# Kernel tuning notes

Hardware: AMD Instinct MI355X
Metric: run time of the kernel (lower is better)

Reference implementation:

```python
import jax, jax.numpy as jnp
import numpy as np

EPS = 1e-6
NUM_HEADS = 16

def rmsnorm(x, w):
    # x: [..., d], w: [d]
    norm = jax.lax.rsqrt(jnp.mean(x * x, axis=-1, keepdims=True) + EPS)
    return w * (x * norm)

def setup_inputs() -> dict:
    key = jax.random.key(0)
    ks = jax.random.split(key, 6)
    B, N, C = 2, 2048, 1024
    H = NUM_HEADS
    hd = C // H
    x = jax.random.normal(ks[0], (B, N, C), dtype=jnp.float32)
    scale = 1.0 / np.sqrt(C)
    qkv_w = jax.random.normal(ks[1], (C, 3 * C), dtype=jnp.float32) * scale
    qkv_b = jnp.zeros((3 * C,), dtype=jnp.float32)
    q_norm_w = jnp.ones((hd,), dtype=jnp.float32)
    k_norm_w = jnp.ones((hd,), dtype=jnp.float32)
    proj_w = jax.random.normal(ks[2], (C, C), dtype=jnp.float32) * scale
    proj_b = jnp.zeros((C,), dtype=jnp.float32)
    return {"x": x, "qkv_w": qkv_w, "qkv_b": qkv_b,
            "q_norm_w": q_norm_w, "k_norm_w": k_norm_w,
            "proj_w": proj_w, "proj_b": proj_b}

def reference(x, qkv_w, qkv_b, q_norm_w, k_norm_w, proj_w, proj_b):
    B, N, C = x.shape
    H = NUM_HEADS
    hd = C // H
    qkv = x @ qkv_w + qkv_b                       # [B,N,3C]
    qkv = qkv.reshape(B, N, 3, H, hd)
    q, k, v = qkv[:, :, 0], qkv[:, :, 1], qkv[:, :, 2]  # [B,N,H,hd]
    q = jnp.transpose(q, (0, 2, 1, 3))            # [B,H,N,hd]
    k = jnp.transpose(k, (0, 2, 1, 3))
    v = jnp.transpose(v, (0, 2, 1, 3))
    q = rmsnorm(q, q_norm_w)
    k = rmsnorm(k, k_norm_w)
    scores = jnp.einsum('bhqd,bhkd->bhqk', q, k) / jnp.sqrt(jnp.float32(hd))
    attn = jax.nn.softmax(scores, axis=-1)
    out = jnp.einsum('bhqk,bhkd->bhqd', attn, v)  # [B,H,N,hd]
    out = jnp.transpose(out, (0, 2, 1, 3)).reshape(B, N, C)
    return out @ proj_w + proj_b
```

## Files before the change

kernel.cpp:

```cpp
#include <hip/hip_runtime.h>

typedef unsigned short u16;
typedef unsigned int u32;
typedef __bf16 bf16x8 __attribute__((ext_vector_type(8)));
typedef float f32x4 __attribute__((ext_vector_type(4)));
typedef unsigned short u16x8 __attribute__((ext_vector_type(8)));
typedef unsigned short u16x4 __attribute__((ext_vector_type(4)));
typedef float f4 __attribute__((ext_vector_type(4)));

__device__ __forceinline__ float bf2f(u16 u) {
    union { unsigned int i; float f; } c; c.i = ((unsigned int)u) << 16; return c.f;
}
__device__ __forceinline__ u16 f2bf(float f) {
    union { float f; unsigned int i; } c; c.f = f;
    unsigned int r = c.i + 0x7FFFu + ((c.i >> 16) & 1u);
    return (u16)(r >> 16);
}
__device__ __forceinline__ u16 f2bf_rtz(float f) {
    union { float f; unsigned int i; } c; c.f = f;
    return (u16)(c.i >> 16);
}
__device__ __forceinline__ float fast_exp2(float x) {
#if __has_builtin(__builtin_amdgcn_exp2f)
    return __builtin_amdgcn_exp2f(x);
#else
    return exp2f(x);
#endif
}
__device__ __forceinline__ void async16(const void* g, void* l) {
    __builtin_amdgcn_global_load_lds(
        (const __attribute__((address_space(1))) u32*)g,
        (__attribute__((address_space(3))) u32*)l, 16, 0, 0);
}

__global__ __launch_bounds__(256) void cast_bf16(
    const float* __restrict__ X, u16* __restrict__ H)
{
    const size_t i = ((size_t)blockIdx.x * 256 + threadIdx.x) * 8;
    u16x8 h;
    #pragma unroll
    for (int e = 0; e < 8; ++e) h[e] = f2bf(X[i + e]);
    *(u16x8*)&H[i] = h;
}

__global__ __launch_bounds__(256) void transpose_cast(
    const float* __restrict__ W, u16* __restrict__ Th, int K, int N)
{
    __shared__ float tile[32][33];
    const int bk = blockIdx.y * 32, bn = blockIdx.x * 32;
    const int tx = threadIdx.x & 31, ty = threadIdx.x >> 5;
    #pragma unroll
    for (int r = ty; r < 32; r += 8)
        tile[r][tx] = W[(size_t)(bk + r) * N + bn + tx];
    __syncthreads();
    #pragma unroll
    for (int r = ty; r < 32; r += 8)
        Th[(size_t)(bn + r) * K + bk + tx] = f2bf(tile[tx][r]);
}

template <int EPI>
__global__ __launch_bounds__(256) void gemm_fused(
    const u16* __restrict__ AH, const u16* __restrict__ BH,
    const float* __restrict__ bias, float* __restrict__ C,
    u16* __restrict__ Qb, u16* __restrict__ Kb, u16* __restrict__ Vt,
    const float* __restrict__ qw, const float* __restrict__ kw,
    int M, int N, int K)
{
    __shared__ __align__(16) u16 AhT[128 * 32];
    __shared__ __align__(16) u16 BhT[128 * 32];
    const int t = threadIdx.x;
    const int bm = blockIdx.y * 128, bn = blockIdx.x * 128;
    const int wave = t >> 6, lane = t & 63;
    const int wm = (wave >> 1) * 64, wn = (wave & 1) * 64;
    const int l15 = lane & 15, quad = lane >> 4;
    const int srow = lane >> 2, scol = (lane & 3) * 8;

    f32x4 acc[4][4];
    const f32x4 zero = {0.0f, 0.0f, 0.0f, 0.0f};
    #pragma unroll
    for (int i = 0; i < 4; ++i)
        #pragma unroll
        for (int j = 0; j < 4; ++j) acc[i][j] = zero;

    for (int k0 = 0; k0 < K; k0 += 32) {
        #pragma unroll
        for (int rr = 0; rr < 2; ++rr) {
            const int r0 = (rr * 4 + wave) * 16;
            const size_t ga = (size_t)(bm + r0 + srow) * K + k0 + scol;
            const size_t gb = (size_t)(bn + r0 + srow) * K + k0 + scol;
            async16(&AH[ga], &AhT[r0 * 32]);
            async16(&BH[gb], &BhT[r0 * 32]);
        }
        __syncthreads();
        bf16x8 ah[4], bh[4];
        #pragma unroll
        for (int i = 0; i < 4; ++i)
            ah[i] = *(const bf16x8*)&AhT[(wm + i * 16 + l15) * 32 + quad * 8];
        #pragma unroll
        for (int j = 0; j < 4; ++j)
            bh[j] = *(const bf16x8*)&BhT[(wn + j * 16 + l15) * 32 + quad * 8];
        #pragma unroll
        for (int i = 0; i < 4; ++i)
            #pragma unroll
            for (int j = 0; j < 4; ++j)
                acc[i][j] = __builtin_amdgcn_mfma_f32_16x16x32_bf16(
                    ah[i], bh[j], acc[i][j], 0, 0, 0);
        __syncthreads();
    }

    if (EPI == 1) {
        #pragma unroll
        for (int j = 0; j < 4; ++j) {
            const int col = bn + wn + j * 16 + l15;
            const float bv = bias[col];
            #pragma unroll
            for (int i = 0; i < 4; ++i) {
                const int row = bm + wm + i * 16 + quad * 4;
                #pragma unroll
                for (int r = 0; r < 4; ++r)
                    C[(size_t)(row + r) * N + col] = acc[i][j][r] + bv;
            }
        }
    } else {
        const int gc0 = bn + wn;
        const int sec = gc0 >> 10;
        const int h = (gc0 & 1023) >> 6;
        const int b = bm >> 11;
        const int bhd = b * 16 + h;
        float bv[4], wj[4];
        #pragma unroll
        for (int j = 0; j < 4; ++j) {
            const int d = j * 16 + l15;
            bv[j] = bias[gc0 + d];
            wj[j] = (sec == 2) ? 0.0f
                  : (sec ? kw[d] : qw[d] * 0.18033688011f);
        }
        if (sec < 2) {
            u16* dst = sec ? Kb : Qb;
            #pragma unroll
            for (int i = 0; i < 4; ++i) {
                float val[4][4];
                float ss[4] = {0.0f, 0.0f, 0.0f, 0.0f};
                #pragma unroll
                for (int j = 0; j < 4; ++j)
                    #pragma unroll
                    for (int r = 0; r < 4; ++r) {
                        val[j][r] = acc[i][j][r] + bv[j];
                        ss[r] += val[j][r] * val[j][r];
                    }
                #pragma unroll
                for (int r = 0; r < 4; ++r) {
                    #pragma unroll
                    for (int m = 1; m < 16; m <<= 1)
                        ss[r] += __shfl_xor(ss[r], m, 64);
                    const float nrm = rsqrtf(ss[r] * 0.015625f + 1e-6f);
                    const int n = (bm + wm + i * 16 + quad * 4 + r) & 2047;
                    const size_t rowb = ((size_t)bhd * 2048 + n) * 64;
                    #pragma unroll
                    for (int j = 0; j < 4; ++j)
                        dst[rowb + j * 16 + l15] = f2bf(val[j][r] * nrm * wj[j]);
                }
            }
        } else {
            #pragma unroll
            for (int i = 0; i < 4; ++i) {
                const int n0 = (bm + wm + i * 16 + quad * 4) & 2047;
                #pragma unroll
                for (int j = 0; j < 4; ++j) {
                    const int d = j * 16 + l15;
                    u16x4 pk;
                    #pragma unroll
                    for (int r = 0; r < 4; ++r)
                        pk[r] = f2bf(acc[i][j][r] + bv[j]);
                    *(u16x4*)&Vt[((size_t)bhd * 64 + d) * 2048 + n0] = pk;
                }
            }
        }
    }
}

__global__ __launch_bounds__(256) void flash_attn_mfma(
    const u16* __restrict__ Qb, const u16* __restrict__ Kb,
    const u16* __restrict__ Vt, u16* __restrict__ Attn)
{
    __shared__ __align__(16) u16 Qlds[128 * 64];
    __shared__ __align__(16) u16 Klds[64 * 64];
    __shared__ __align__(16) u16 Vlds[64 * 64];
    __shared__ u16 Plds[128][72];

    const int t = threadIdx.x;
    const int qt = blockIdx.x;
    const int bh = blockIdx.y;
    const int n0 = qt * 128;
    const size_t qbase = ((size_t)bh * 2048 + n0) * 64;
    const size_t kbase = (size_t)bh * 2048 * 64;
    const size_t vbase = (size_t)bh * 64 * 2048;
    const int wave = t >> 6, lane = t & 63;
    const int l15 = lane & 15, quad = lane >> 4;
    const int srow8 = lane >> 3;
    const int sgrp = lane & 7;

    #pragma unroll
    for (int c = 0; c < 4; ++c) {
        const int r0 = wave * 32 + c * 8;
        const int row = r0 + srow8;
        const int gg = sgrp ^ (row & 7);
        async16(&Qb[qbase + (size_t)row * 64 + gg * 8], &Qlds[r0 * 64]);
    }
    __syncthreads();

    int kofs[4][2];
    #pragma unroll
    for (int nt = 0; nt < 4; ++nt) {
        const int row = nt * 16 + l15;
        kofs[nt][0] = row * 64 + ((quad ^ (row & 7)) * 8);
        kofs[nt][1] = row * 64 + (((quad + 4) ^ (row & 7)) * 8);
    }
    bf16x8 qf[2][2];
    #pragma unroll
    for (int qs = 0; qs < 2; ++qs) {
        const int row = wave * 32 + qs * 16 + l15;
        qf[qs][0] = *(const bf16x8*)&Qlds[row * 64 + ((quad ^ (row & 7)) * 8)];
        qf[qs][1] = *(const bf16x8*)&Qlds[row * 64 + (((quad + 4) ^ (row & 7)) * 8)];
    }

    f32x4 o[2][4];
    const f32x4 zero = {0.0f, 0.0f, 0.0f, 0.0f};
    #pragma unroll
    for (int qs = 0; qs < 2; ++qs)
        #pragma unroll
        for (int dt = 0; dt < 4; ++dt) o[qs][dt] = zero;
    float lsum[2][4] = {};

    for (int kt = 0; kt < 32; ++kt) {
        __syncthreads();
        #pragma unroll
        for (int cc = 0; cc < 2; ++cc) {
            const int r0 = (wave + cc * 4) * 8;
            const int row = r0 + srow8;
            const int gg = sgrp ^ (row & 7);
            async16(&Kb[kbase + (size_t)(kt * 64 + row) * 64 + gg * 8],
                    &Klds[r0 * 64]);
            async16(&Vt[vbase + (size_t)row * 2048 + kt * 64 + gg * 8],
                    &Vlds[r0 * 64]);
        }
        __syncthreads();

        f32x4 s[2][4];
        #pragma unroll
        for (int nt = 0; nt < 4; ++nt) {
            bf16x8 kf0 = *(const bf16x8*)&Klds[kofs[nt][0]];
            bf16x8 kf1 = *(const bf16x8*)&Klds[kofs[nt][1]];
            #pragma unroll
            for (int qs = 0; qs < 2; ++qs) {
                s[qs][nt] = zero;
                s[qs][nt] = __builtin_amdgcn_mfma_f32_16x16x32_bf16(
                    qf[qs][0], kf0, s[qs][nt], 0, 0, 0);
                s[qs][nt] = __builtin_amdgcn_mfma_f32_16x16x32_bf16(
                    qf[qs][1], kf1, s[qs][nt], 0, 0, 0);
            }
        }

        #pragma unroll
        for (int qs = 0; qs < 2; ++qs) {
            const int prow = wave * 32 + qs * 16 + quad * 4;
            #pragma unroll
            for (int nt = 0; nt < 4; ++nt)
                #pragma unroll
                for (int r = 0; r < 4; ++r) {
                    const float p = fast_exp2(s[qs][nt][r]);
                    lsum[qs][r] += p;
                    Plds[prow + r][nt * 16 + l15] = f2bf_rtz(p);
                }
        }

        bf16x8 pf[2][2];
        #pragma unroll
        for (int qs = 0; qs < 2; ++qs) {
            const int prow = wave * 32 + qs * 16 + l15;
            pf[qs][0] = *(const bf16x8*)&Plds[prow][quad * 8];
            pf[qs][1] = *(const bf16x8*)&Plds[prow][quad * 8 + 32];
        }

        #pragma unroll
        for (int dt = 0; dt < 4; ++dt) {
            bf16x8 vf0 = *(const bf16x8*)&Vlds[kofs[dt][0]];
            bf16x8 vf1 = *(const bf16x8*)&Vlds[kofs[dt][1]];
            #pragma unroll
            for (int qs = 0; qs < 2; ++qs) {
                o[qs][dt] = __builtin_amdgcn_mfma_f32_16x16x32_bf16(
                    pf[qs][0], vf0, o[qs][dt], 0, 0, 0);
                o[qs][dt] = __builtin_amdgcn_mfma_f32_16x16x32_bf16(
                    pf[qs][1], vf1, o[qs][dt], 0, 0, 0);
            }
        }
    }

    #pragma unroll
    for (int qs = 0; qs < 2; ++qs)
        #pragma unroll
        for (int r = 0; r < 4; ++r) {
            #pragma unroll
            for (int m = 1; m < 16; m <<= 1)
                lsum[qs][r] += __shfl_xor(lsum[qs][r], m, 64);
        }
    const size_t obase =
        ((size_t)(bh >> 4) * 2048 + n0) * 1024 + (bh & 15) * 64;
    #pragma unroll
    for (int qs = 0; qs < 2; ++qs)
        #pragma unroll
        for (int r = 0; r < 4; ++r) {
            const float inv = 1.0f / lsum[qs][r];
            const size_t rbase =
                obase + (size_t)(wave * 32 + qs * 16 + quad * 4 + r) * 1024;
            #pragma unroll
            for (int dt = 0; dt < 4; ++dt)
                Attn[rbase + dt * 16 + l15] = f2bf(o[qs][dt][r] * inv);
        }
}

extern "C" void kernel_launch(void* const* d_in, const int* in_sizes, int n_in,
                              void* d_out, int out_size, void* d_ws, size_t ws_size,
                              hipStream_t stream)
{
    const float* x      = (const float*)d_in[0];
    const float* qkv_w  = (const float*)d_in[1];
    const float* qkv_b  = (const float*)d_in[2];
    const float* q_nw   = (const float*)d_in[3];
    const float* k_nw   = (const float*)d_in[4];
    const float* proj_w = (const float*)d_in[5];
    const float* proj_b = (const float*)d_in[6];
    float* out = (float*)d_out;

    char* ws = (char*)d_ws;
    u16* AttnB = (u16*)ws;
    u16* qwT   = (u16*)(ws + 8388608);
    u16* pwT   = (u16*)(ws + 14680064);
    u16* Xb    = (u16*)(ws + 16777216);
    u16* QbB   = (u16*)(ws + 25165824);
    u16* KbB   = (u16*)(ws + 33554432);
    u16* VtB   = (u16*)(ws + 41943040);
    (void)in_sizes; (void)n_in; (void)out_size;
    if (ws_size < 50331648u) return;

    cast_bf16<<<dim3(2048), 256, 0, stream>>>(x, Xb);
    transpose_cast<<<dim3(3072 / 32, 1024 / 32), 256, 0, stream>>>(
        qkv_w, qwT, 1024, 3072);
    transpose_cast<<<dim3(1024 / 32, 1024 / 32), 256, 0, stream>>>(
        proj_w, pwT, 1024, 1024);
    gemm_fused<0><<<dim3(3072 / 128, 4096 / 128), 256, 0, stream>>>(
        Xb, qwT, qkv_b, nullptr, QbB, KbB, VtB, q_nw, k_nw, 4096, 3072, 1024);
    flash_attn_mfma<<<dim3(16, 32), 256, 0, stream>>>(QbB, KbB, VtB, AttnB);
    gemm_fused<1><<<dim3(1024 / 128, 4096 / 128), 256, 0, stream>>>(
        AttnB, pwT, proj_b, out, nullptr, nullptr, nullptr, nullptr, nullptr,
        4096, 1024, 1024);
}
```

Measured before the change: 226.2 us.

## Split attention over two key halves and shrink projection GEMM tiles

Flash attention now splits the key sequence into two halves along a new grid z dimension. Each half writes unnormalized fp32 partial outputs and row sums, and a new combine kernel adds them, normalizes and casts to bf16. This doubles the number of attention blocks so the 256 CUs get more concurrent work. The projection GEMM is split out with a 64x128 tile, doubling its block count for the same reason. The cost is extra fp32 partial-output traffic, one more kernel launch and a larger workspace. The combine is only correct because the softmax does no running-max rescaling, which appears to rely on normalized q/k keeping scores bounded.

```diff
diff --git a/kernel.cpp b/kernel.cpp
--- a/kernel.cpp
+++ b/kernel.cpp
@@ -58,14 +58,13 @@
         Th[(size_t)(bn + r) * K + bk + tx] = f2bf(tile[tx][r]);
 }
 
-template <int EPI>
-__global__ __launch_bounds__(256) void gemm_fused(
+__global__ __launch_bounds__(256) void gemm_qkv(
     const u16* __restrict__ AH, const u16* __restrict__ BH,
-    const float* __restrict__ bias, float* __restrict__ C,
+    const float* __restrict__ bias,
     u16* __restrict__ Qb, u16* __restrict__ Kb, u16* __restrict__ Vt,
-    const float* __restrict__ qw, const float* __restrict__ kw,
-    int M, int N, int K)
-{
+    const float* __restrict__ qw, const float* __restrict__ kw)
+{
+    const int M = 4096, N = 3072, K = 1024; (void)M; (void)N;
     __shared__ __align__(16) u16 AhT[128 * 32];
     __shared__ __align__(16) u16 BhT[128 * 32];
     const int t = threadIdx.x;
@@ -108,80 +107,129 @@
         __syncthreads();
     }
 
-    if (EPI == 1) {
-        #pragma unroll
-        for (int j = 0; j < 4; ++j) {
-            const int col = bn + wn + j * 16 + l15;
-            const float bv = bias[col];
-            #pragma unroll
-            for (int i = 0; i < 4; ++i) {
-                const int row = bm + wm + i * 16 + quad * 4;
+    const int gc0 = bn + wn;
+    const int sec = gc0 >> 10;
+    const int h = (gc0 & 1023) >> 6;
+    const int b = bm >> 11;
+    const int bhd = b * 16 + h;
+    float bv[4], wj[4];
+    #pragma unroll
+    for (int j = 0; j < 4; ++j) {
+        const int d = j * 16 + l15;
+        bv[j] = bias[gc0 + d];
+        wj[j] = (sec == 2) ? 0.0f : (sec ? kw[d] : qw[d] * 0.18033688011f);
+    }
+    if (sec < 2) {
+        u16* dst = sec ? Kb : Qb;
+        #pragma unroll
+        for (int i = 0; i < 4; ++i) {
+            float val[4][4];
+            float ss[4] = {0.0f, 0.0f, 0.0f, 0.0f};
+            #pragma unroll
+            for (int j = 0; j < 4; ++j)
+                #pragma unroll
+                for (int r = 0; r < 4; ++r) {
+                    val[j][r] = acc[i][j][r] + bv[j];
+                    ss[r] += val[j][r] * val[j][r];
+                }
+            #pragma unroll
+            for (int r = 0; r < 4; ++r) {
+                #pragma unroll
+                for (int m = 1; m < 16; m <<= 1)
+                    ss[r] += __shfl_xor(ss[r], m, 64);
+                const float nrm = rsqrtf(ss[r] * 0.015625f + 1e-6f);
+                const int n = (bm + wm + i * 16 + quad * 4 + r) & 2047;
+                const size_t rowb = ((size_t)bhd * 2048 + n) * 64;
+                #pragma unroll
+                for (int j = 0; j < 4; ++j)
+                    dst[rowb + j * 16 + l15] = f2bf(val[j][r] * nrm * wj[j]);
+            }
+        }
+    } else {
+        #pragma unroll
+        for (int i = 0; i < 4; ++i) {
+            const int n0 = (bm + wm + i * 16 + quad * 4) & 2047;
+            #pragma unroll
+            for (int j = 0; j < 4; ++j) {
+                const int d = j * 16 + l15;
+                u16x4 pk;
                 #pragma unroll
                 for (int r = 0; r < 4; ++r)
-                    C[(size_t)(row + r) * N + col] = acc[i][j][r] + bv;
+                    pk[r] = f2bf(acc[i][j][r] + bv[j]);
+                *(u16x4*)&Vt[((size_t)bhd * 64 + d) * 2048 + n0] = pk;
             }
         }
-    } else {
-        const int gc0 = bn + wn;
-        const int sec = gc0 >> 10;
-        const int h = (gc0 & 1023) >> 6;
-        const int b = bm >> 11;
-        const int bhd = b * 16 + h;
-        float bv[4], wj[4];
-        #pragma unroll
-        for (int j = 0; j < 4; ++j) {
-            const int d = j * 16 + l15;
-            bv[j] = bias[gc0 + d];
-            wj[j] = (sec == 2) ? 0.0f
-                  : (sec ? kw[d] : qw[d] * 0.18033688011f);
-        }
-        if (sec < 2) {
-            u16* dst = sec ? Kb : Qb;
-            #pragma unroll
-            for (int i = 0; i < 4; ++i) {
-                float val[4][4];
-                float ss[4] = {0.0f, 0.0f, 0.0f, 0.0f};
-                #pragma unroll
-                for (int j = 0; j < 4; ++j)
-                    #pragma unroll
-                    for (int r = 0; r < 4; ++r) {
-                        val[j][r] = acc[i][j][r] + bv[j];
-                        ss[r] += val[j][r] * val[j][r];
-                    }
-                #pragma unroll
-                for (int r = 0; r < 4; ++r) {
-                    #pragma unroll
-                    for (int m = 1; m < 16; m <<= 1)
-                        ss[r] += __shfl_xor(ss[r], m, 64);
-                    const float nrm = rsqrtf(ss[r] * 0.015625f + 1e-6f);
-                    const int n = (bm + wm + i * 16 + quad * 4 + r) & 2047;
-                    const size_t rowb = ((size_t)bhd * 2048 + n) * 64;
-                    #pragma unroll
-                    for (int j = 0; j < 4; ++j)
-                        dst[rowb + j * 16 + l15] = f2bf(val[j][r] * nrm * wj[j]);
-                }
-            }
-        } else {
-            #pragma unroll
-            for (int i = 0; i < 4; ++i) {
-                const int n0 = (bm + wm + i * 16 + quad * 4) & 2047;
-                #pragma unroll
-                for (int j = 0; j < 4; ++j) {
-                    const int d = j * 16 + l15;
-                    u16x4 pk;
-                    #pragma unroll
-                    for (int r = 0; r < 4; ++r)
-                        pk[r] = f2bf(acc[i][j][r] + bv[j]);
-                    *(u16x4*)&Vt[((size_t)bhd * 64 + d) * 2048 + n0] = pk;
-                }
-            }
+    }
+}
+
+__global__ __launch_bounds__(256) void gemm_proj(
+    const u16* __restrict__ AH, const u16* __restrict__ BH,
+    const float* __restrict__ bias, float* __restrict__ C)
+{
+    const int N = 1024, K = 1024;
+    __shared__ __align__(16) u16 AhT[64 * 32];
+    __shared__ __align__(16) u16 BhT[128 * 32];
+    const int t = threadIdx.x;
+    const int bm = blockIdx.y * 64, bn = blockIdx.x * 128;
+    const int wave = t >> 6, lane = t & 63;
+    const int l15 = lane & 15, quad = lane >> 4;
+    const int srow = lane >> 2, scol = (lane & 3) * 8;
+
+    f32x4 acc[4][2];
+    const f32x4 zero = {0.0f, 0.0f, 0.0f, 0.0f};
+    #pragma unroll
+    for (int i = 0; i < 4; ++i)
+        #pragma unroll
+        for (int j = 0; j < 2; ++j) acc[i][j] = zero;
+
+    for (int k0 = 0; k0 < K; k0 += 32) {
+        {
+            const int r0 = wave * 16;
+            async16(&AH[(size_t)(bm + r0 + srow) * K + k0 + scol],
+                    &AhT[r0 * 32]);
+        }
+        #pragma unroll
+        for (int cc = 0; cc < 2; ++cc) {
+            const int r0 = (wave * 2 + cc) * 16;
+            async16(&BH[(size_t)(bn + r0 + srow) * K + k0 + scol],
+                    &BhT[r0 * 32]);
+        }
+        __syncthreads();
+        bf16x8 ah[4], bh[2];
+        #pragma unroll
+        for (int i = 0; i < 4; ++i)
+            ah[i] = *(const bf16x8*)&AhT[(i * 16 + l15) * 32 + quad * 8];
+        #pragma unroll
+        for (int j = 0; j < 2; ++j)
+            bh[j] = *(const bf16x8*)
+                &BhT[(wave * 32 + j * 16 + l15) * 32 + quad * 8];
+        #pragma unroll
+        for (int i = 0; i < 4; ++i)
+            #pragma unroll
+            for (int j = 0; j < 2; ++j)
+                acc[i][j] = __builtin_amdgcn_mfma_f32_16x16x32_bf16(
+                    ah[i], bh[j], acc[i][j], 0, 0, 0);
+        __syncthreads();
+    }
+
+    #pragma unroll
+    for (int j = 0; j < 2; ++j) {
+        const int col = bn + wave * 32 + j * 16 + l15;
+        const float bv = bias[col];
+        #pragma unroll
+        for (int i = 0; i < 4; ++i) {
+            const int row = bm + i * 16 + quad * 4;
+            #pragma unroll
+            for (int r = 0; r < 4; ++r)
+                C[(size_t)(row + r) * N + col] = acc[i][j][r] + bv;
         }
     }
 }
 
 __global__ __launch_bounds__(256) void flash_attn_mfma(
     const u16* __restrict__ Qb, const u16* __restrict__ Kb,
-    const u16* __restrict__ Vt, u16* __restrict__ Attn)
+    const u16* __restrict__ Vt, float* __restrict__ Opart,
+    float* __restrict__ Lpart)
 {
     __shared__ __align__(16) u16 Qlds[128 * 64];
     __shared__ __align__(16) u16 Klds[64 * 64];
@@ -191,6 +239,7 @@
     const int t = threadIdx.x;
     const int qt = blockIdx.x;
     const int bh = blockIdx.y;
+    const int z = blockIdx.z;
     const int n0 = qt * 128;
     const size_t qbase = ((size_t)bh * 2048 + n0) * 64;
     const size_t kbase = (size_t)bh * 2048 * 64;
@@ -232,16 +281,17 @@
         for (int dt = 0; dt < 4; ++dt) o[qs][dt] = zero;
     float lsum[2][4] = {};
 
-    for (int kt = 0; kt < 32; ++kt) {
+    for (int kt = 0; kt < 16; ++kt) {
+        const int ktG = z * 16 + kt;
         __syncthreads();
         #pragma unroll
         for (int cc = 0; cc < 2; ++cc) {
             const int r0 = (wave + cc * 4) * 8;
             const int row = r0 + srow8;
             const int gg = sgrp ^ (row & 7);
-            async16(&Kb[kbase + (size_t)(kt * 64 + row) * 64 + gg * 8],
+            async16(&Kb[kbase + (size_t)(ktG * 64 + row) * 64 + gg * 8],
                     &Klds[r0 * 64]);
-            async16(&Vt[vbase + (size_t)row * 2048 + kt * 64 + gg * 8],
+            async16(&Vt[vbase + (size_t)row * 2048 + ktG * 64 + gg * 8],
                     &Vlds[r0 * 64]);
         }
         __syncthreads();
@@ -304,19 +354,43 @@
             for (int m = 1; m < 16; m <<= 1)
                 lsum[qs][r] += __shfl_xor(lsum[qs][r], m, 64);
         }
+    const int b = bh >> 4, h = bh & 15;
     const size_t obase =
-        ((size_t)(bh >> 4) * 2048 + n0) * 1024 + (bh & 15) * 64;
+        ((size_t)z * 4096 + b * 2048 + n0) * 1024 + h * 64;
+    const size_t lbase = (size_t)z * 32 * 2048 + (size_t)bh * 2048 + n0;
     #pragma unroll
     for (int qs = 0; qs < 2; ++qs)
         #pragma unroll
         for (int r = 0; r < 4; ++r) {
-            const float inv = 1.0f / lsum[qs][r];
-            const size_t rbase =
-                obase + (size_t)(wave * 32 + qs * 16 + quad * 4 + r) * 1024;
+            const int rofs = wave * 32 + qs * 16 + quad * 4 + r;
+            if (l15 == 0) Lpart[lbase + rofs] = lsum[qs][r];
+            const size_t rbase = obase + (size_t)rofs * 1024;
             #pragma unroll
             for (int dt = 0; dt < 4; ++dt)
-                Attn[rbase + dt * 16 + l15] = f2bf(o[qs][dt][r] * inv);
-        }
+                Opart[rbase + dt * 16 + l15] = o[qs][dt][r];
+        }
+}
+
+__global__ __launch_bounds__(256) void attn_combine(
+    const float* __restrict__ Opart, const float* __restrict__ Lpart,
+    u16* __restrict__ Attn)
+{
+    const int row = blockIdx.x;
+    const int t = threadIdx.x;
+    const int col = t * 4;
+    const int b = row >> 11, n = row & 2047;
+    const int h = col >> 6;
+    const int bh = b * 16 + h;
+    const float l0 = Lpart[(size_t)bh * 2048 + n];
+    const float l1 = Lpart[65536 + (size_t)bh * 2048 + n];
+    const float inv = 1.0f / (l0 + l1);
+    const size_t idx = (size_t)row * 1024 + col;
+    f4 o0 = *(const f4*)&Opart[idx];
+    f4 o1 = *(const f4*)&Opart[4194304 + idx];
+    u16x4 pk;
+    #pragma unroll
+    for (int e = 0; e < 4; ++e) pk[e] = f2bf((o0[e] + o1[e]) * inv);
+    *(u16x4*)&Attn[idx] = pk;
 }
 
 extern "C" void kernel_launch(void* const* d_in, const int* in_sizes, int n_in,
@@ -333,25 +407,28 @@
     float* out = (float*)d_out;
 
     char* ws = (char*)d_ws;
-    u16* AttnB = (u16*)ws;
-    u16* qwT   = (u16*)(ws + 8388608);
-    u16* pwT   = (u16*)(ws + 14680064);
-    u16* Xb    = (u16*)(ws + 16777216);
-    u16* QbB   = (u16*)(ws + 25165824);
-    u16* KbB   = (u16*)(ws + 33554432);
-    u16* VtB   = (u16*)(ws + 41943040);
+    u16* AttnB  = (u16*)ws;
+    u16* qwT    = (u16*)(ws + 8388608);
+    u16* pwT    = (u16*)(ws + 14680064);
+    u16* Xb     = (u16*)(ws + 16777216);
+    float* Lp   = (float*)(ws + 16777216);
+    u16* QbB    = (u16*)(ws + 25165824);
+    u16* KbB    = (u16*)(ws + 33554432);
+    u16* VtB    = (u16*)(ws + 41943040);
+    float* Op   = (float*)(ws + 50331648);
     (void)in_sizes; (void)n_in; (void)out_size;
-    if (ws_size < 50331648u) return;
+    if (ws_size < 83886080u) return;
 
     cast_bf16<<<dim3(2048), 256, 0, stream>>>(x, Xb);
     transpose_cast<<<dim3(3072 / 32, 1024 / 32), 256, 0, stream>>>(
         qkv_w, qwT, 1024, 3072);
     transpose_cast<<<dim3(1024 / 32, 1024 / 32), 256, 0, stream>>>(
         proj_w, pwT, 1024, 1024);
-    gemm_fused<0><<<dim3(3072 / 128, 4096 / 128), 256, 0, stream>>>(
-        Xb, qwT, qkv_b, nullptr, QbB, KbB, VtB, q_nw, k_nw, 4096, 3072, 1024);
-    flash_attn_mfma<<<dim3(16, 32), 256, 0, stream>>>(QbB, KbB, VtB, AttnB);
-    gemm_fused<1><<<dim3(1024 / 128, 4096 / 128), 256, 0, stream>>>(
-        AttnB, pwT, proj_b, out, nullptr, nullptr, nullptr, nullptr, nullptr,
-        4096, 1024, 1024);
-}
+    gemm_qkv<<<dim3(3072 / 128, 4096 / 128), 256, 0, stream>>>(
+        Xb, qwT, qkv_b, QbB, KbB, VtB, q_nw, k_nw);
+    flash_attn_mfma<<<dim3(16, 32, 2), 256, 0, stream>>>(
+        QbB, KbB, VtB, Op, Lp);
+    attn_combine<<<dim3(4096), 256, 0, stream>>>(Op, Lp, AttnB);
+    gemm_proj<<<dim3(1024 / 128, 4096 / 64), 256, 0, stream>>>(
+        AttnB, pwT, proj_b, out);
+}
```

After: 211.8 us. 6.4% less time.
